# Optimization experiments

Hardware: AMD Instinct MI355X
Metric: run time of the kernel (lower is better)

Reference implementation:

```python
import jax, jax.numpy as jnp
import numpy as np
from jax.ops import segment_sum

N_NODES = 50000
N_EDGES = 150000
IN_FEATS = 512
OUT_FEATS = 512


def setup_inputs() -> dict:
    key = jax.random.key(0)
    k1, k2, k3, k4 = jax.random.split(key, 4)
    x = jax.random.normal(k1, (N_NODES, IN_FEATS), dtype=jnp.float32)
    src = jax.random.randint(k2, (N_EDGES,), 0, N_NODES, dtype=jnp.int64)
    dst = jax.random.randint(k3, (N_EDGES,), 0, N_NODES, dtype=jnp.int64)
    # Xavier-uniform init like reset_parameters
    limit = float(np.sqrt(6.0 / (IN_FEATS + OUT_FEATS)))
    W = jax.random.uniform(k4, (IN_FEATS, OUT_FEATS), dtype=jnp.float32,
                           minval=-limit, maxval=limit)
    b = jnp.zeros((OUT_FEATS,), dtype=jnp.float32)
    return {"x": x, "src": src, "dst": dst, "W": W, "b": b}


def reference(x, src, dst, W, b):
    # DGL GraphConv with norm='both':
    #   out = relu( D_dst^{-1/2} A D_src^{-1/2} X W + b )
    # Dropout is identity in eval mode (training=False).
    ones = jnp.ones((src.shape[0],), dtype=x.dtype)
    deg_out = segment_sum(ones, src, num_segments=N_NODES)  # source out-degree
    deg_in = segment_sum(ones, dst, num_segments=N_NODES)   # dest in-degree
    norm_src = jnp.where(deg_out > 0, deg_out, 1.0) ** -0.5  # [N]
    norm_dst = jnp.where(deg_in > 0, deg_in, 1.0) ** -0.5    # [N]

    h = x * norm_src[:, None]                         # [N, in]
    agg = segment_sum(h[src], dst, num_segments=N_NODES)  # scatter-add over edges
    agg = agg * norm_dst[:, None]                     # [N, in]
    out = agg @ W + b                                 # [N, out]
    return jax.nn.relu(out)
```

## Files before the change

### kernel.cpp

```cpp
#include <hip/hip_runtime.h>
#include <hip/hip_bf16.h>

#define N_NODES 50000
#define N_PAD   50048
#define N_EDGES 150000
#define F 512
#define BM 128
#define BN 128
#define BK 64
#define NBLK 196
#define NWG  1564

typedef __attribute__((ext_vector_type(4))) float f32x4;
typedef __attribute__((ext_vector_type(4))) unsigned int u32x4;
typedef __attribute__((ext_vector_type(2))) unsigned int u32x2;

__device__ __forceinline__ unsigned short f2bf(float f) {
    unsigned int u = __float_as_uint(f);
    return (unsigned short)((u + 0x7fffu + ((u >> 16) & 1u)) >> 16);
}
__device__ __forceinline__ unsigned int pack2(float a, float b) {
    return (unsigned int)f2bf(a) | ((unsigned int)f2bf(b) << 16);
}
__device__ __forceinline__ void gload16(const void* g, void* l) {
    __builtin_amdgcn_global_load_lds(
        (const __attribute__((address_space(1))) unsigned int*)g,
        (__attribute__((address_space(3))) unsigned int*)l, 16, 0, 0);
}

__global__ void __launch_bounds__(256) crd_deg(const int* __restrict__ src,
                                               const int* __restrict__ dst,
                                               int* __restrict__ hist) {
    int e = blockIdx.x * 256 + threadIdx.x;
    if (e < N_EDGES) {
        atomicAdd(&hist[src[e]], 1);
        atomicAdd(&hist[N_NODES + dst[e]], 1);
    }
}

__global__ void __launch_bounds__(256) crd_norm(const int* __restrict__ hist,
                                                float* __restrict__ norms) {
    int i = blockIdx.x * 256 + threadIdx.x;
    if (i < 2 * N_NODES) {
        int d = hist[i];
        norms[i] = rsqrtf((float)(d > 0 ? d : 1));
    }
}

__global__ void __launch_bounds__(256) crd_bsum(const int* __restrict__ hist_in,
                                                int* __restrict__ bsum) {
    __shared__ int s[256];
    int t = threadIdx.x;
    int i = blockIdx.x * 256 + t;
    s[t] = (i < N_NODES) ? hist_in[i] : 0;
    __syncthreads();
    #pragma unroll
    for (int o = 128; o > 0; o >>= 1) {
        if (t < o) s[t] += s[t + o];
        __syncthreads();
    }
    if (t == 0) bsum[blockIdx.x] = s[0];
}

__global__ void __launch_bounds__(256) crd_bscan(const int* __restrict__ bsum,
                                                 int* __restrict__ bsumoff) {
    __shared__ int s[256];
    int t = threadIdx.x;
    int v = (t < NBLK) ? bsum[t] : 0;
    s[t] = v;
    __syncthreads();
    #pragma unroll
    for (int d = 1; d < 256; d <<= 1) {
        int add = (t >= d) ? s[t - d] : 0;
        __syncthreads();
        s[t] += add;
        __syncthreads();
    }
    if (t < NBLK) bsumoff[t] = s[t] - v;
}

__global__ void __launch_bounds__(256) crd_escan(const int* __restrict__ hist_in,
                                                 const int* __restrict__ bsumoff,
                                                 int* __restrict__ off,
                                                 int* __restrict__ cursor) {
    __shared__ int s[256];
    int t = threadIdx.x;
    int i = blockIdx.x * 256 + t;
    int v = (i < N_NODES) ? hist_in[i] : 0;
    s[t] = v;
    __syncthreads();
    #pragma unroll
    for (int d = 1; d < 256; d <<= 1) {
        int add = (t >= d) ? s[t - d] : 0;
        __syncthreads();
        s[t] += add;
        __syncthreads();
    }
    int excl = s[t] - v + bsumoff[blockIdx.x];
    if (i < N_NODES) { off[i] = excl; cursor[i] = excl; }
    if (i == N_NODES - 1) off[N_NODES] = excl + v;
}

__global__ void __launch_bounds__(256) crd_place(const int* __restrict__ src,
                                                 const int* __restrict__ dst,
                                                 int* __restrict__ cursor,
                                                 int* __restrict__ sorted) {
    int e = blockIdx.x * 256 + threadIdx.x;
    if (e < N_EDGES) {
        int slot = atomicAdd(&cursor[dst[e]], 1);
        sorted[slot] = src[e];
    }
}

__global__ void __launch_bounds__(256) crd_wt(const float* __restrict__ W,
                                              unsigned short* __restrict__ Wt) {
    int idx = blockIdx.x * 256 + threadIdx.x;
    int n = idx >> 9, k = idx & 511;
    Wt[idx] = f2bf(W[k * F + n]);
}

__global__ void __launch_bounds__(256) crd_gather(const float* __restrict__ x,
                                                  const int* __restrict__ sorted,
                                                  const int* __restrict__ off,
                                                  const float* __restrict__ norms,
                                                  unsigned short* __restrict__ aggb) {
    int gw = (blockIdx.x * 256 + threadIdx.x) >> 6;
    int lane = threadIdx.x & 63;
    int wid = gw >> 1, half = gw & 1;
    if (wid >= N_PAD) return;
    f32x4 a = {0.f,0.f,0.f,0.f}, b = a;
    if (wid < N_NODES) {
        int e0 = off[wid], e1 = off[wid + 1];
        const float* xh = x + half * 256;
        int e = e0;
        for (; e + 1 < e1; e += 2) {
            int s0 = sorted[e], s1 = sorted[e + 1];
            float ns0 = norms[s0], ns1 = norms[s1];
            a += ((const f32x4*)(xh + (size_t)s0 * F))[lane] * ns0;
            b += ((const f32x4*)(xh + (size_t)s1 * F))[lane] * ns1;
        }
        if (e < e1) {
            int s = sorted[e];
            a += ((const f32x4*)(xh + (size_t)s * F))[lane] * norms[s];
        }
        float nd = norms[N_NODES + wid];
        a = (a + b) * nd;
    }
    u32x2 w;
    w.x = pack2(a.x, a.y); w.y = pack2(a.z, a.w);
    *(u32x2*)(aggb + (size_t)wid * F + half * 256 + lane * 4) = w;
}

__global__ void __launch_bounds__(256, 3) crd_gemm(const unsigned short* __restrict__ aggb,
                                                   const unsigned short* __restrict__ Wt,
                                                   const float* __restrict__ bias,
                                                   float* __restrict__ out) {
    __shared__ __align__(16) unsigned short lA[8 * BM * 8];
    __shared__ __align__(16) unsigned short lB[8 * BN * 8];
    const int tid = threadIdx.x;
    int bid = blockIdx.x;
    int xcd = bid & 7, lid = bid >> 3;
    int swz = (xcd < 4 ? xcd * 196 : 784 + (xcd - 4) * 195) + lid;
    const int rowbase = (swz >> 2) * BM;
    const int nbase = (swz & 3) * BN;
    const int lane = tid & 63;
    const int wave = tid >> 6;
    const int wm = wave >> 1, wn = wave & 1;
    const int g = lane >> 4, r = lane & 15;

    f32x4 acc[4][4];
    #pragma unroll
    for (int i = 0; i < 4; ++i)
        #pragma unroll
        for (int j = 0; j < 4; ++j) acc[i][j] = (f32x4){0.f, 0.f, 0.f, 0.f};

    for (int ks = 0; ks < F / BK; ++ks) {
        #pragma unroll
        for (int j = 0; j < 4; ++j) {
            int gg = (wave * 4 + j) * 64 + lane;
            int k8 = gg >> 7, row = gg & 127;
            gload16(aggb + (size_t)(rowbase + row) * F + ks * BK + k8 * 8,
                    &lA[(size_t)(wave * 4 + j) * 64 * 8]);
        }
        #pragma unroll
        for (int j = 0; j < 4; ++j) {
            int gg = (wave * 4 + j) * 64 + lane;
            int k8 = gg >> 7, n = gg & 127;
            gload16(Wt + (size_t)(nbase + n) * F + ks * BK + k8 * 8,
                    &lB[(size_t)(wave * 4 + j) * 64 * 8]);
        }
        __syncthreads();
        #pragma unroll
        for (int kk = 0; kk < 2; ++kk) {
            int k8 = kk * 4 + g;
            u32x4 af[4], bfr[4];
            #pragma unroll
            for (int mi = 0; mi < 4; ++mi)
                af[mi] = *(const u32x4*)&lA[(k8 * BM + wm * 64 + mi * 16 + r) * 8];
            #pragma unroll
            for (int ni = 0; ni < 4; ++ni)
                bfr[ni] = *(const u32x4*)&lB[(k8 * BN + wn * 64 + ni * 16 + r) * 8];
            #pragma unroll
            for (int mi = 0; mi < 4; ++mi)
                #pragma unroll
                for (int ni = 0; ni < 4; ++ni)
                    asm("v_mfma_f32_16x16x32_bf16 %0, %1, %2, %0"
                        : "+v"(acc[mi][ni]) : "v"(bfr[ni]), "v"(af[mi]));
        }
        __syncthreads();
    }
    #pragma unroll
    for (int mi = 0; mi < 4; ++mi) {
        int row = rowbase + wm * 64 + mi * 16 + r;
        if (row < N_NODES) {
            #pragma unroll
            for (int ni = 0; ni < 4; ++ni) {
                int c0 = nbase + wn * 64 + ni * 16 + g * 4;
                f32x4 bv = *(const f32x4*)(bias + c0);
                f32x4 v = acc[mi][ni] + bv;
                v.x = fmaxf(v.x, 0.f); v.y = fmaxf(v.y, 0.f);
                v.z = fmaxf(v.z, 0.f); v.w = fmaxf(v.w, 0.f);
                *(f32x4*)(out + (size_t)row * F + c0) = v;
            }
        }
    }
}

extern "C" void kernel_launch(void* const* d_in, const int* in_sizes, int n_in,
                              void* d_out, int out_size, void* d_ws, size_t ws_size,
                              hipStream_t stream) {
    const float* x = (const float*)d_in[0];
    const int* src = (const int*)d_in[1];
    const int* dst = (const int*)d_in[2];
    const float* W = (const float*)d_in[3];
    const float* bias = (const float*)d_in[4];
    float* out = (float*)d_out;

    float* norms = (float*)d_ws;
    int* hist = (int*)(norms + 2 * N_NODES);
    int* off = hist + 2 * N_NODES;
    int* cursor = off + N_NODES + 1;
    int* sorted = cursor + N_NODES;
    int* bsum = sorted + N_EDGES;
    int* bsumoff = bsum + NBLK;
    unsigned short* Wt = (unsigned short*)
        (((uintptr_t)(bsumoff + NBLK) + 63) & ~(uintptr_t)63);
    unsigned short* aggb = Wt + (size_t)F * F;
    size_t need = (size_t)((char*)(aggb + (size_t)N_PAD * F) - (char*)d_ws);
    if (ws_size < need) {
        hipMemsetAsync(d_out, 0, (size_t)out_size * sizeof(float), stream);
        return;
    }

    hipMemsetAsync(hist, 0, 2 * N_NODES * sizeof(int), stream);
    crd_deg<<<(N_EDGES + 255) / 256, 256, 0, stream>>>(src, dst, hist);
    crd_norm<<<(2 * N_NODES + 255) / 256, 256, 0, stream>>>(hist, norms);
    crd_wt<<<(F * F) / 256, 256, 0, stream>>>(W, Wt);
    crd_bsum<<<NBLK, 256, 0, stream>>>(hist + N_NODES, bsum);
    crd_bscan<<<1, 256, 0, stream>>>(bsum, bsumoff);
    crd_escan<<<NBLK, 256, 0, stream>>>(hist + N_NODES, bsumoff, off, cursor);
    crd_place<<<(N_EDGES + 255) / 256, 256, 0, stream>>>(src, dst, cursor, sorted);
    crd_gather<<<N_PAD / 2, 256, 0, stream>>>(x, sorted, off, norms, aggb);
    crd_gemm<<<NWG, 256, 0, stream>>>(aggb, Wt, bias, out);
}
```

Measured before the change: 165.1 us.

## Double-buffer GEMM LDS tiles with BK=32 to overlap loads and MFMA

Halves the K tile to 32 and adds a second LDS buffer so the next tile's global-to-LDS loads are issued before the MFMA work on the current tile. This aims to hide global load latency behind compute in the aggregated-features GEMM. In exchange there are twice as many K iterations and barriers. Relying on one barrier per iteration, with no explicit wait on the async loads, risks load/compute ordering problems.

```diff
diff --git a/kernel.cpp b/kernel.cpp
--- a/kernel.cpp
+++ b/kernel.cpp
@@ -7,7 +7,7 @@
 #define F 512
 #define BM 128
 #define BN 128
-#define BK 64
+#define BK 32
 #define NBLK 196
 #define NWG  1564
 
@@ -155,8 +155,8 @@
                                                    const unsigned short* __restrict__ Wt,
                                                    const float* __restrict__ bias,
                                                    float* __restrict__ out) {
-    __shared__ __align__(16) unsigned short lA[8 * BM * 8];
-    __shared__ __align__(16) unsigned short lB[8 * BN * 8];
+    __shared__ __align__(16) unsigned short lA[2][4 * BM * 8];
+    __shared__ __align__(16) unsigned short lB[2][4 * BN * 8];
     const int tid = threadIdx.x;
     int bid = blockIdx.x;
     int xcd = bid & 7, lid = bid >> 3;
@@ -174,32 +174,36 @@
         #pragma unroll
         for (int j = 0; j < 4; ++j) acc[i][j] = (f32x4){0.f, 0.f, 0.f, 0.f};
 
+#define STAGE(B, KS) do { \
+    _Pragma("unroll") \
+    for (int j_ = 0; j_ < 2; ++j_) { \
+        int gg = j_ * 256 + tid;                  \
+        int k8 = gg >> 7, rw = gg & 127; \
+        gload16(aggb + (size_t)(rowbase + rw) * F + (KS) * BK + k8 * 8, \
+                &lA[B][(j_ * 256 + wave * 64) * 8]); \
+    } \
+    _Pragma("unroll") \
+    for (int j_ = 0; j_ < 2; ++j_) { \
+        int gg = j_ * 256 + tid; \
+        int k8 = gg >> 7, nn = gg & 127; \
+        gload16(Wt + (size_t)(nbase + nn) * F + (KS) * BK + k8 * 8, \
+                &lB[B][(j_ * 256 + wave * 64) * 8]); \
+    } \
+} while (0)
+
+    STAGE(0, 0);
+    __syncthreads();
     for (int ks = 0; ks < F / BK; ++ks) {
-        #pragma unroll
-        for (int j = 0; j < 4; ++j) {
-            int gg = (wave * 4 + j) * 64 + lane;
-            int k8 = gg >> 7, row = gg & 127;
-            gload16(aggb + (size_t)(rowbase + row) * F + ks * BK + k8 * 8,
-                    &lA[(size_t)(wave * 4 + j) * 64 * 8]);
-        }
-        #pragma unroll
-        for (int j = 0; j < 4; ++j) {
-            int gg = (wave * 4 + j) * 64 + lane;
-            int k8 = gg >> 7, n = gg & 127;
-            gload16(Wt + (size_t)(nbase + n) * F + ks * BK + k8 * 8,
-                    &lB[(size_t)(wave * 4 + j) * 64 * 8]);
-        }
-        __syncthreads();
-        #pragma unroll
-        for (int kk = 0; kk < 2; ++kk) {
-            int k8 = kk * 4 + g;
+        int buf = ks & 1;
+        if (ks + 1 < F / BK) STAGE(buf ^ 1, ks + 1);
+        {
             u32x4 af[4], bfr[4];
             #pragma unroll
             for (int mi = 0; mi < 4; ++mi)
-                af[mi] = *(const u32x4*)&lA[(k8 * BM + wm * 64 + mi * 16 + r) * 8];
+                af[mi] = *(const u32x4*)&lA[buf][(g * BM + wm * 64 + mi * 16 + r) * 8];
             #pragma unroll
             for (int ni = 0; ni < 4; ++ni)
-                bfr[ni] = *(const u32x4*)&lB[(k8 * BN + wn * 64 + ni * 16 + r) * 8];
+                bfr[ni] = *(const u32x4*)&lB[buf][(g * BN + wn * 64 + ni * 16 + r) * 8];
             #pragma unroll
             for (int mi = 0; mi < 4; ++mi)
                 #pragma unroll
@@ -209,6 +213,8 @@
         }
         __syncthreads();
     }
+#undef STAGE
+
     #pragma unroll
     for (int mi = 0; mi < 4; ++mi) {
         int row = rowbase + wm * 64 + mi * 16 + r;
```

New measurement: 168.1 us. Within noise of the previous version (+1.9%).

## Fuse prep kernels and retile GEMM to 256x64 blocks with occupancy 4

Applied to the files above, without the earlier changes.

Merges the degree histogram with the W transpose/convert kernel and the norm computation with the block-sum kernel, removing two launches. The GEMM tile changes from 128x128 to 256x64, so each wave now owns a 64-row strip against the full 64-column B tile. The launch-bounds occupancy hint rises from 3 to 4, and the XCD swizzle and row padding are adjusted to match. The new tile shape loads more A per block and less W, and the higher occupancy hint may squeeze registers.

```diff
diff --git a/kernel.cpp b/kernel.cpp
--- a/kernel.cpp
+++ b/kernel.cpp
@@ -2,14 +2,15 @@
 #include <hip/hip_bf16.h>
 
 #define N_NODES 50000
-#define N_PAD   50048
+#define N_PAD   50176
 #define N_EDGES 150000
 #define F 512
-#define BM 128
-#define BN 128
+#define BM 256
+#define BN 64
 #define BK 64
 #define NBLK 196
-#define NWG  1564
+#define NWG  1568
+#define DEGB 586
 
 typedef __attribute__((ext_vector_type(4))) float f32x4;
 typedef __attribute__((ext_vector_type(4))) unsigned int u32x4;
@@ -28,38 +29,45 @@
         (__attribute__((address_space(3))) unsigned int*)l, 16, 0, 0);
 }
 
-__global__ void __launch_bounds__(256) crd_deg(const int* __restrict__ src,
-                                               const int* __restrict__ dst,
-                                               int* __restrict__ hist) {
-    int e = blockIdx.x * 256 + threadIdx.x;
-    if (e < N_EDGES) {
-        atomicAdd(&hist[src[e]], 1);
-        atomicAdd(&hist[N_NODES + dst[e]], 1);
-    }
-}
-
-__global__ void __launch_bounds__(256) crd_norm(const int* __restrict__ hist,
-                                                float* __restrict__ norms) {
-    int i = blockIdx.x * 256 + threadIdx.x;
+__global__ void __launch_bounds__(256) crd_deg_wt(const int* __restrict__ src,
+                                                  const int* __restrict__ dst,
+                                                  int* __restrict__ hist,
+                                                  const float* __restrict__ W,
+                                                  unsigned short* __restrict__ Wt) {
+    int b = blockIdx.x;
+    if (b < DEGB) {
+        int e = b * 256 + threadIdx.x;
+        if (e < N_EDGES) {
+            atomicAdd(&hist[src[e]], 1);
+            atomicAdd(&hist[N_NODES + dst[e]], 1);
+        }
+    } else {
+        int idx = (b - DEGB) * 256 + threadIdx.x;
+        int n = idx >> 9, k = idx & 511;
+        Wt[idx] = f2bf(W[k * F + n]);
+    }
+}
+
+__global__ void __launch_bounds__(256) crd_norm_bsum(const int* __restrict__ hist,
+                                                     float* __restrict__ norms,
+                                                     int* __restrict__ bsum) {
+    __shared__ int s[256];
+    int b = blockIdx.x, t = threadIdx.x;
+    int i = b * 256 + t;
     if (i < 2 * N_NODES) {
         int d = hist[i];
         norms[i] = rsqrtf((float)(d > 0 ? d : 1));
     }
-}
-
-__global__ void __launch_bounds__(256) crd_bsum(const int* __restrict__ hist_in,
-                                                int* __restrict__ bsum) {
-    __shared__ int s[256];
-    int t = threadIdx.x;
-    int i = blockIdx.x * 256 + t;
-    s[t] = (i < N_NODES) ? hist_in[i] : 0;
-    __syncthreads();
-    #pragma unroll
-    for (int o = 128; o > 0; o >>= 1) {
-        if (t < o) s[t] += s[t + o];
-        __syncthreads();
-    }
-    if (t == 0) bsum[blockIdx.x] = s[0];
+    if (b < NBLK) {
+        s[t] = (i < N_NODES) ? hist[N_NODES + i] : 0;
+        __syncthreads();
+        #pragma unroll
+        for (int o = 128; o > 0; o >>= 1) {
+            if (t < o) s[t] += s[t + o];
+            __syncthreads();
+        }
+        if (t == 0) bsum[b] = s[0];
+    }
 }
 
 __global__ void __launch_bounds__(256) crd_bscan(const int* __restrict__ bsum,
@@ -110,13 +118,6 @@
         int slot = atomicAdd(&cursor[dst[e]], 1);
         sorted[slot] = src[e];
     }
-}
-
-__global__ void __launch_bounds__(256) crd_wt(const float* __restrict__ W,
-                                              unsigned short* __restrict__ Wt) {
-    int idx = blockIdx.x * 256 + threadIdx.x;
-    int n = idx >> 9, k = idx & 511;
-    Wt[idx] = f2bf(W[k * F + n]);
 }
 
 __global__ void __launch_bounds__(256) crd_gather(const float* __restrict__ x,
@@ -151,7 +152,7 @@
     *(u32x2*)(aggb + (size_t)wid * F + half * 256 + lane * 4) = w;
 }
 
-__global__ void __launch_bounds__(256, 3) crd_gemm(const unsigned short* __restrict__ aggb,
+__global__ void __launch_bounds__(256, 4) crd_gemm(const unsigned short* __restrict__ aggb,
                                                    const unsigned short* __restrict__ Wt,
                                                    const float* __restrict__ bias,
                                                    float* __restrict__ out) {
@@ -159,13 +160,11 @@
     __shared__ __align__(16) unsigned short lB[8 * BN * 8];
     const int tid = threadIdx.x;
     int bid = blockIdx.x;
-    int xcd = bid & 7, lid = bid >> 3;
-    int swz = (xcd < 4 ? xcd * 196 : 784 + (xcd - 4) * 195) + lid;
-    const int rowbase = (swz >> 2) * BM;
-    const int nbase = (swz & 3) * BN;
+    int swz = (bid & 7) * 196 + (bid >> 3);
+    const int rowbase = (swz >> 3) * BM;
+    const int nbase = (swz & 7) * BN;
     const int lane = tid & 63;
     const int wave = tid >> 6;
-    const int wm = wave >> 1, wn = wave & 1;
     const int g = lane >> 4, r = lane & 15;
 
     f32x4 acc[4][4];
@@ -176,18 +175,18 @@
 
     for (int ks = 0; ks < F / BK; ++ks) {
         #pragma unroll
-        for (int j = 0; j < 4; ++j) {
-            int gg = (wave * 4 + j) * 64 + lane;
-            int k8 = gg >> 7, row = gg & 127;
+        for (int j = 0; j < 8; ++j) {
+            int gg = j * 256 + tid;
+            int k8 = gg >> 8, row = gg & 255;
             gload16(aggb + (size_t)(rowbase + row) * F + ks * BK + k8 * 8,
-                    &lA[(size_t)(wave * 4 + j) * 64 * 8]);
-        }
-        #pragma unroll
-        for (int j = 0; j < 4; ++j) {
-            int gg = (wave * 4 + j) * 64 + lane;
-            int k8 = gg >> 7, n = gg & 127;
+                    &lA[(size_t)(j * 256 + wave * 64) * 8]);
+        }
+        #pragma unroll
+        for (int j = 0; j < 2; ++j) {
+            int gg = j * 256 + tid;
+            int k8 = gg >> 6, n = gg & 63;
             gload16(Wt + (size_t)(nbase + n) * F + ks * BK + k8 * 8,
-                    &lB[(size_t)(wave * 4 + j) * 64 * 8]);
+                    &lB[(size_t)(j * 256 + wave * 64) * 8]);
         }
         __syncthreads();
         #pragma unroll
@@ -196,10 +195,10 @@
             u32x4 af[4], bfr[4];
             #pragma unroll
             for (int mi = 0; mi < 4; ++mi)
-                af[mi] = *(const u32x4*)&lA[(k8 * BM + wm * 64 + mi * 16 + r) * 8];
+                af[mi] = *(const u32x4*)&lA[(k8 * BM + wave * 64 + mi * 16 + r) * 8];
             #pragma unroll
             for (int ni = 0; ni < 4; ++ni)
-                bfr[ni] = *(const u32x4*)&lB[(k8 * BN + wn * 64 + ni * 16 + r) * 8];
+                bfr[ni] = *(const u32x4*)&lB[(k8 * BN + ni * 16 + r) * 8];
             #pragma unroll
             for (int mi = 0; mi < 4; ++mi)
                 #pragma unroll
@@ -211,11 +210,11 @@
     }
     #pragma unroll
     for (int mi = 0; mi < 4; ++mi) {
-        int row = rowbase + wm * 64 + mi * 16 + r;
+        int row = rowbase + wave * 64 + mi * 16 + r;
         if (row < N_NODES) {
             #pragma unroll
             for (int ni = 0; ni < 4; ++ni) {
-                int c0 = nbase + wn * 64 + ni * 16 + g * 4;
+                int c0 = nbase + ni * 16 + g * 4;
                 f32x4 bv = *(const f32x4*)(bias + c0);
                 f32x4 v = acc[mi][ni] + bv;
                 v.x = fmaxf(v.x, 0.f); v.y = fmaxf(v.y, 0.f);
@@ -253,10 +252,8 @@
     }
 
     hipMemsetAsync(hist, 0, 2 * N_NODES * sizeof(int), stream);
-    crd_deg<<<(N_EDGES + 255) / 256, 256, 0, stream>>>(src, dst, hist);
-    crd_norm<<<(2 * N_NODES + 255) / 256, 256, 0, stream>>>(hist, norms);
-    crd_wt<<<(F * F) / 256, 256, 0, stream>>>(W, Wt);
-    crd_bsum<<<NBLK, 256, 0, stream>>>(hist + N_NODES, bsum);
+    crd_deg_wt<<<DEGB + (F * F) / 256, 256, 0, stream>>>(src, dst, hist, W, Wt);
+    crd_norm_bsum<<<391, 256, 0, stream>>>(hist, norms, bsum);
     crd_bscan<<<1, 256, 0, stream>>>(bsum, bsumoff);
     crd_escan<<<NBLK, 256, 0, stream>>>(hist + N_NODES, bsumoff, off, cursor);
     crd_place<<<(N_EDGES + 255) / 256, 256, 0, stream>>>(src, dst, cursor, sorted);
```

After: 185.6 us. 1.12x slower.
